# Kernel optimization log

Measured on AMD Instinct MI355X. Metric: run time of the kernel, lower is better.

## Reference

```python
import jax, jax.numpy as jnp
import numpy as np


def _gelu(x):
    # torch F.gelu default = exact (erf) gelu
    return jax.nn.gelu(x, approximate=False)


def _gatv2(x, src, dst, Wl, bl, Wr, br, att, bout, n):
    """PyG GATv2Conv, concat=False (mean over heads), negative_slope=0.2."""
    H, C = att.shape
    xl = (x @ Wl + bl).reshape(n, H, C)  # source-side transform (messages)
    xr = (x @ Wr + br).reshape(n, H, C)  # target-side transform
    e = jax.nn.leaky_relu(xl[src] + xr[dst], 0.2)      # [E,H,C]
    logits = jnp.einsum('ehc,hc->eh', e, att)          # [E,H]
    # segment softmax over incoming edges of each target node
    m = jax.ops.segment_max(logits, dst, num_segments=n)
    m = jnp.where(jnp.isfinite(m), m, 0.0)
    p = jnp.exp(logits - m[dst])
    den = jax.ops.segment_sum(p, dst, num_segments=n)
    alpha = p / (den[dst] + 1e-16)
    out = jax.ops.segment_sum(alpha[:, :, None] * xl[src], dst, num_segments=n)  # [N,H,C]
    return out.mean(axis=1) + bout


def _gnorm(x, w, b, ms):
    """PyG GraphNorm with a single graph (batch == zeros)."""
    mu = x.mean(axis=0, keepdims=True)
    o = x - ms * mu
    var = (o * o).mean(axis=0, keepdims=True)
    return w * o / jnp.sqrt(var + 1e-5) + b


def setup_inputs() -> dict:
    N, E, HID, LAT = 50000, 300000, 128, 256
    key = jax.random.key(0)
    ks = iter(jax.random.split(key, 48))

    def rn(shape, s=0.05):
        return jax.random.normal(next(ks), shape, jnp.float32) * s

    d = {}
    d['z_g'] = rn((1, LAT), 1.0)
    d['edge_index'] = jax.random.randint(next(ks), (2, E), 0, N, dtype=jnp.int32)
    d['template_vertices'] = rn((N, 3), 1.0)
    d['W_ne1'] = rn((3, HID)); d['b_ne1'] = jnp.zeros((HID,))
    d['W_ne2'] = rn((HID, HID)); d['b_ne2'] = jnp.zeros((HID,))
    d['W_s1'] = rn((LAT, HID)); d['b_s1'] = jnp.zeros((HID,))
    d['W_s2'] = rn((HID, HID)); d['b_s2'] = jnp.zeros((HID,))
    for i, h in ((1, 2), (2, 2), (3, 1)):
        d[f'Wl{i}'] = rn((HID, h * HID)); d[f'bl{i}'] = jnp.zeros((h * HID,))
        d[f'Wr{i}'] = rn((HID, h * HID)); d[f'br{i}'] = jnp.zeros((h * HID,))
        d[f'att{i}'] = rn((h, HID)); d[f'bo{i}'] = jnp.zeros((HID,))
        d[f'gn{i}_w'] = jnp.ones((HID,)); d[f'gn{i}_b'] = jnp.zeros((HID,))
        d[f'gn{i}_ms'] = jnp.ones((HID,))
    d['W_h1'] = rn((HID, HID // 2)); d['b_h1'] = jnp.zeros((HID // 2,))
    d['W_h2'] = rn((HID // 2, 3)); d['b_h2'] = jnp.zeros((3,))
    return d


def reference(z_g, edge_index, template_vertices,
              W_ne1, b_ne1, W_ne2, b_ne2, W_s1, b_s1, W_s2, b_s2,
              Wl1, bl1, Wr1, br1, att1, bo1, gn1_w, gn1_b, gn1_ms,
              Wl2, bl2, Wr2, br2, att2, bo2, gn2_w, gn2_b, gn2_ms,
              Wl3, bl3, Wr3, br3, att3, bo3, gn3_w, gn3_b, gn3_ms,
              W_h1, b_h1, W_h2, b_h2):
    n = template_vertices.shape[0]
    sl = jnp.arange(n, dtype=edge_index.dtype)
    src = jnp.concatenate([edge_index[0], sl])  # GATv2Conv add_self_loops=True
    dst = jnp.concatenate([edge_index[1], sl])
    # node embedding + broadcast style (eval mode -> dropout is identity)
    x = _gelu(template_vertices @ W_ne1 + b_ne1) @ W_ne2 + b_ne2
    style = _gelu(z_g @ W_s1 + b_s1) @ W_s2 + b_s2   # [1, hidden]
    x = x + style
    x = _gelu(_gnorm(_gatv2(x, src, dst, Wl1, bl1, Wr1, br1, att1, bo1, n), gn1_w, gn1_b, gn1_ms))
    x = _gelu(_gnorm(_gatv2(x, src, dst, Wl2, bl2, Wr2, br2, att2, bo2, n), gn2_w, gn2_b, gn2_ms))
    x = _gelu(_gnorm(_gatv2(x, src, dst, Wl3, bl3, Wr3, br3, att3, bo3, n), gn3_w, gn3_b, gn3_ms))
    displacement = _gelu(x @ W_h1 + b_h1) @ W_h2 + b_h2   # [n, 3]
    return displacement
```

## Files before the change

kernel.cpp:

```cpp
#include <hip/hip_runtime.h>
#include <hip/hip_fp16.h>
#include <math.h>

#define DEVINL __device__ __forceinline__

using bf16x8 = __attribute__((ext_vector_type(8))) short;
using f32x4  = __attribute__((ext_vector_type(4))) float;
using u16x4  = __attribute__((ext_vector_type(4))) unsigned short;

DEVINL float gelu_f(float v) { return 0.5f * v * (1.0f + erff(v * 0.7071067811865475f)); }
DEVINL float lrelu_f(float v) { return v > 0.0f ? v : 0.2f * v; }
DEVINL unsigned short f2bf(float f) {
    union { float f; unsigned u; } c; c.f = f;
    unsigned r = c.u + 0x7fffu + ((c.u >> 16) & 1u);
    return (unsigned short)(r >> 16);
}
DEVINL float bf2f(unsigned short s) {
    union { unsigned u; float f; } c; c.u = (unsigned)s << 16;
    return c.f;
}
DEVINL unsigned short f2h(float f) {
    __half h = __float2half_rn(f);
    return *(unsigned short*)&h;
}
DEVINL void gl_lds16(const void* g, void* l) {
    __builtin_amdgcn_global_load_lds(
        (const __attribute__((address_space(1))) unsigned*)g,
        (__attribute__((address_space(3))) unsigned*)l, 16, 0, 0);
}
DEVINL void unp8h(const unsigned short* p, float* v) {
    uint4 u = *(const uint4*)p;
    __half2 h0 = *(__half2*)&u.x, h1 = *(__half2*)&u.y;
    __half2 h2 = *(__half2*)&u.z, h3 = *(__half2*)&u.w;
    float2 f0 = __half22float2(h0), f1 = __half22float2(h1);
    float2 f2 = __half22float2(h2), f3 = __half22float2(h3);
    v[0] = f0.x; v[1] = f0.y; v[2] = f1.x; v[3] = f1.y;
    v[4] = f2.x; v[5] = f2.y; v[6] = f3.x; v[7] = f3.y;
}

__global__ void style_k(const float* __restrict__ zg, const float* __restrict__ W1,
                        const float* __restrict__ b1, const float* __restrict__ W2,
                        const float* __restrict__ b2, float* __restrict__ style) {
    __shared__ float s1[128];
    int j = threadIdx.x;
    float a = b1[j];
    for (int k = 0; k < 256; k++) a = fmaf(zg[k], W1[k * 128 + j], a);
    s1[j] = gelu_f(a);
    __syncthreads();
    float o = b2[j];
    for (int k = 0; k < 128; k++) o = fmaf(s1[k], W2[k * 128 + j], o);
    style[j] = o;
}

__global__ void ne1_k(const float* __restrict__ tv, const float* __restrict__ W,
                      const float* __restrict__ b, float* __restrict__ h1, int Nn) {
    int idx = blockIdx.x * blockDim.x + threadIdx.x;
    if (idx >= Nn * 128) return;
    int n = idx >> 7, c = idx & 127;
    float o = fmaf(tv[n * 3 + 0], W[c],
              fmaf(tv[n * 3 + 1], W[128 + c],
              fmaf(tv[n * 3 + 2], W[256 + c], b[c])));
    h1[idx] = gelu_f(o);
}

struct PrepArgs {
    const float* src[8];
    unsigned short* dst;
    int dstoff[8];
    int off[9];
    int shift[8];
};
__global__ void prep_k(PrepArgs a) {
    int idx = blockIdx.x * 256 + threadIdx.x;
    if (idx >= a.off[8]) return;
    int s = 0;
    while (idx >= a.off[s + 1]) s++;
    int e = idx - a.off[s];
    int sh = a.shift[s];
    int k = e >> sh, j = e & ((1 << sh) - 1);
    float w = a.src[s][e];
    unsigned short hi = f2bf(w);
    unsigned short lo = f2bf(w - bf2f(hi));
    int c = j >> 4, lr = j & 15;
    int s2 = k >> 5, lk = (k >> 3) & 3, i = k & 7;
    int lane = lk * 16 + lr;
    size_t base = (size_t)a.dstoff[s] + (size_t)c * 4096 + s2 * 512 + lane * 8 + i;
    a.dst[base] = hi;
    a.dst[base + 2048] = lo;
}

template <int OUT, int EPI, bool DUAL, typename OutT>
__global__ __launch_bounds__(256) void mfma_lin_k(
    const float* __restrict__ xin,
    const unsigned short* __restrict__ WT0, const float* __restrict__ b0,
    const unsigned short* __restrict__ WT1, const float* __restrict__ b1,
    const float* __restrict__ style,
    OutT* __restrict__ out0, OutT* __restrict__ out1, int Nn) {
    constexpr int CPM = OUT / 16;
    constexpr int NCH = (DUAL ? 2 : 1) * CPM;
    __shared__ uint4 buf[2][512];
    int t = threadIdx.x;
    int wave = t >> 6, lane = t & 63;
    int lr = lane & 15, lk = lane >> 4;
    int base = blockIdx.x * 128 + wave * 32;
    int r0 = base + lr, r1 = base + 16 + lr;
    int cr0 = min(r0, Nn - 1), cr1 = min(r1, Nn - 1);

    bf16x8 xh[2][4], xlo[2][4];
#pragma unroll
    for (int rr = 0; rr < 2; rr++) {
        const float* px = xin + (size_t)(rr ? cr1 : cr0) * 128;
#pragma unroll
        for (int s = 0; s < 4; s++) {
            const float4* p4 = (const float4*)(px + s * 32 + lk * 8);
            float4 a = p4[0], b = p4[1];
            float v[8] = {a.x, a.y, a.z, a.w, b.x, b.y, b.z, b.w};
            bf16x8 h, l;
#pragma unroll
            for (int i = 0; i < 8; i++) {
                unsigned short hb = f2bf(v[i]);
                h[i] = (short)hb;
                l[i] = (short)f2bf(v[i] - bf2f(hb));
            }
            xh[rr][s] = h;
            xlo[rr][s] = l;
        }
    }

    auto stage = [&](int c, int bsel) {
        const unsigned short* Wt = (DUAL && c >= CPM) ? WT1 : WT0;
        int cc = (DUAL && c >= CPM) ? c - CPM : c;
        const char* g = (const char*)(Wt + (size_t)cc * 4096);
        char* l = (char*)&buf[bsel][0];
        gl_lds16(g + t * 16, l + wave * 1024);
        gl_lds16(g + 4096 + t * 16, l + 4096 + wave * 1024);
    };

    stage(0, 0);
    for (int c = 0; c < NCH; ++c) {
        int cur = c & 1;
        bool pre = (c + 1 < NCH);
        if (pre) stage(c + 1, cur ^ 1);
        if (pre) asm volatile("s_waitcnt vmcnt(2)" ::: "memory");
        else     asm volatile("s_waitcnt vmcnt(0)" ::: "memory");
        __builtin_amdgcn_s_barrier();

        int m = (DUAL && c >= CPM) ? 1 : 0;
        int j0 = (c - m * CPM) * 16;
        const float* bias = m ? b1 : b0;
        OutT* out = m ? out1 : out0;
        const bf16x8* W = (const bf16x8*)&buf[cur][0];

        f32x4 acc0 = {0.f, 0.f, 0.f, 0.f}, acc1 = {0.f, 0.f, 0.f, 0.f};
#pragma unroll
        for (int s = 0; s < 4; ++s) {
            bf16x8 wh = W[s * 64 + lane];
            bf16x8 wl = W[256 + s * 64 + lane];
            acc0 = __builtin_amdgcn_mfma_f32_16x16x32_bf16(wh, xh[0][s], acc0, 0, 0, 0);
            acc0 = __builtin_amdgcn_mfma_f32_16x16x32_bf16(wh, xlo[0][s], acc0, 0, 0, 0);
            acc0 = __builtin_amdgcn_mfma_f32_16x16x32_bf16(wl, xh[0][s], acc0, 0, 0, 0);
            acc1 = __builtin_amdgcn_mfma_f32_16x16x32_bf16(wh, xh[1][s], acc1, 0, 0, 0);
            acc1 = __builtin_amdgcn_mfma_f32_16x16x32_bf16(wh, xlo[1][s], acc1, 0, 0, 0);
            acc1 = __builtin_amdgcn_mfma_f32_16x16x32_bf16(wl, xh[1][s], acc1, 0, 0, 0);
        }
        int j = j0 + lk * 4;
        float o0[4], o1[4];
#pragma unroll
        for (int i = 0; i < 4; i++) {
            float bb = bias[j + i];
            if (EPI == 1) bb += style[j + i];
            float v0 = acc0[i] + bb, v1 = acc1[i] + bb;
            if (EPI == 2) { v0 = gelu_f(v0); v1 = gelu_f(v1); }
            o0[i] = v0; o1[i] = v1;
        }
        if constexpr (sizeof(OutT) == 2) {
            u16x4 s0 = {f2h(o0[0]), f2h(o0[1]), f2h(o0[2]), f2h(o0[3])};
            u16x4 s1v = {f2h(o1[0]), f2h(o1[1]), f2h(o1[2]), f2h(o1[3])};
            if (r0 < Nn) *(u16x4*)((unsigned short*)out + (size_t)r0 * OUT + j) = s0;
            if (r1 < Nn) *(u16x4*)((unsigned short*)out + (size_t)r1 * OUT + j) = s1v;
        } else {
            if (r0 < Nn) { f32x4 v = {o0[0], o0[1], o0[2], o0[3]}; *(f32x4*)((float*)out + (size_t)r0 * OUT + j) = v; }
            if (r1 < Nn) { f32x4 v = {o1[0], o1[1], o1[2], o1[3]}; *(f32x4*)((float*)out + (size_t)r1 * OUT + j) = v; }
        }
        __builtin_amdgcn_s_barrier();
    }
}

__global__ void count_k(const int* __restrict__ dst, int* __restrict__ counts, int E, int EP) {
    int e = blockIdx.x * blockDim.x + threadIdx.x;
    if (e >= EP) return;
    int d = (e < E) ? dst[e] : (e - E);
    atomicAdd(&counts[d], 1);
}

__global__ void tile_sum_k(const int* __restrict__ counts, int* __restrict__ tsum, int Nn) {
    int i = blockIdx.x * 256 + threadIdx.x;
    int v = (i < Nn) ? counts[i] : 0;
    int lane = threadIdx.x & 63, wave = threadIdx.x >> 6;
#pragma unroll
    for (int off = 1; off < 64; off <<= 1) v += __shfl_xor(v, off, 64);
    __shared__ int red[4];
    if (lane == 0) red[wave] = v;
    __syncthreads();
    if (threadIdx.x == 0) tsum[blockIdx.x] = red[0] + red[1] + red[2] + red[3];
}

__global__ void tile_scan_k(const int* __restrict__ tsum, int* __restrict__ toff,
                            int ntiles, int* __restrict__ rowptr, int Nn, int total) {
    __shared__ int s[256];
    int t = threadIdx.x;
    int v = (t < ntiles) ? tsum[t] : 0;
    s[t] = v;
    __syncthreads();
    for (int off = 1; off < 256; off <<= 1) {
        int a = (t >= off) ? s[t - off] : 0;
        __syncthreads();
        s[t] += a;
        __syncthreads();
    }
    if (t < ntiles) toff[t] = s[t] - v;
    if (t == 0) rowptr[Nn] = total;
}

__global__ void tile_write_k(const int* __restrict__ counts, const int* __restrict__ toff,
                             int* __restrict__ rowptr, int Nn) {
    int i = blockIdx.x * 256 + threadIdx.x;
    int t = threadIdx.x;
    int v = (i < Nn) ? counts[i] : 0;
    __shared__ int s[256];
    s[t] = v;
    __syncthreads();
    for (int off = 1; off < 256; off <<= 1) {
        int a = (t >= off) ? s[t - off] : 0;
        __syncthreads();
        s[t] += a;
        __syncthreads();
    }
    if (i < Nn) rowptr[i] = toff[blockIdx.x] + s[t] - v;
}

__global__ void fill_k(const int* __restrict__ src, const int* __restrict__ dst,
                       const int* __restrict__ rowptr, int* __restrict__ fillc,
                       int* __restrict__ col, int E, int EP) {
    int e = blockIdx.x * blockDim.x + threadIdx.x;
    if (e >= EP) return;
    int d = (e < E) ? dst[e] : (e - E);
    int s = (e < E) ? src[e] : (e - E);
    int pos = atomicAdd(&fillc[d], 1);
    col[rowptr[d] + pos] = s;
}

template <int H>
__global__ __launch_bounds__(256) void gat_gather_k(
    const unsigned short* __restrict__ xl, const unsigned short* __restrict__ xr,
    const float* __restrict__ att, const float* __restrict__ bo,
    const int* __restrict__ rowptr, const int* __restrict__ col,
    float* __restrict__ y, int Nn) {
    constexpr int NPB = (H == 2) ? 2 : 4;
    int w = threadIdx.x >> 6;
    int slot = (H == 2) ? (w >> 1) : w;
    int h = (H == 2) ? (w & 1) : 0;
    int lane = threadIdx.x & 63;
    int g = lane >> 4, sub = lane & 15;
    constexpr int HC = H * 128;
    int n = blockIdx.x * NPB + slot;
    bool act = n < Nn;
    int nn = act ? n : 0;

    float xrv[8], av[8];
    unp8h(xr + (size_t)nn * HC + h * 128 + sub * 8, xrv);
    const float* ap = att + h * 128 + sub * 8;
#pragma unroll
    for (int i = 0; i < 8; i++) av[i] = ap[i];

    float den = 0.f;
    float acc[8] = {0.f, 0.f, 0.f, 0.f, 0.f, 0.f, 0.f, 0.f};
    int beg = act ? rowptr[n] : 0, endp = act ? rowptr[n + 1] : 0;

    for (int k0 = beg; k0 < endp; k0 += 4) {
        int k = k0 + g;
        bool ev = k < endp;
        int s = col[ev ? k : beg];
        float v[8];
        unp8h(xl + (size_t)s * HC + h * 128 + sub * 8, v);
        float p = lrelu_f(v[0] + xrv[0]) * av[0];
#pragma unroll
        for (int i = 1; i < 8; i++) p = fmaf(lrelu_f(v[i] + xrv[i]), av[i], p);
        p += __shfl_xor(p, 1, 64);
        p += __shfl_xor(p, 2, 64);
        p += __shfl_xor(p, 4, 64);
        p += __shfl_xor(p, 8, 64);
        float pe = ev ? __expf(p) : 0.f;
        den += pe;
#pragma unroll
        for (int i = 0; i < 8; i++) acc[i] = fmaf(pe, v[i], acc[i]);
    }
#pragma unroll
    for (int off = 16; off <= 32; off <<= 1) {
        den += __shfl_xor(den, off, 64);
#pragma unroll
        for (int j = 0; j < 8; j++) acc[j] += __shfl_xor(acc[j], off, 64);
    }
    float inv = 1.0f / (den + 1e-16f);

    if constexpr (H == 1) {
        if (act && g == 0) {
            const float* bp = bo + sub * 8;
            f32x4 o0 = {acc[0] * inv + bp[0], acc[1] * inv + bp[1], acc[2] * inv + bp[2], acc[3] * inv + bp[3]};
            f32x4 o1 = {acc[4] * inv + bp[4], acc[5] * inv + bp[5], acc[6] * inv + bp[6], acc[7] * inv + bp[7]};
            *(f32x4*)(y + (size_t)n * 128 + sub * 8) = o0;
            *(f32x4*)(y + (size_t)n * 128 + sub * 8 + 4) = o1;
        }
    } else {
        __shared__ float sh[NPB][2][128];
        if (g == 0) {
#pragma unroll
            for (int j = 0; j < 8; j++) sh[slot][h][sub * 8 + j] = acc[j] * inv;
        }
        __syncthreads();
        int t = threadIdx.x;
        int slot2 = t >> 7, c = t & 127;
        int n2 = blockIdx.x * NPB + slot2;
        if (n2 < Nn)
            y[(size_t)n2 * 128 + c] = (sh[slot2][0][c] + sh[slot2][1][c]) * 0.5f + bo[c];
    }
}

__global__ void gn_stats_k(const float* __restrict__ y, float* __restrict__ stats, int Nn) {
    int c = threadIdx.x;
    int per = (Nn + gridDim.x - 1) / gridDim.x;
    int n0 = blockIdx.x * per, n1 = min(n0 + per, Nn);
    float s = 0.f, s2 = 0.f;
    for (int n = n0; n < n1; n++) {
        float v = y[(size_t)n * 128 + c];
        s += v;
        s2 = fmaf(v, v, s2);
    }
    atomicAdd(&stats[c], s);
    atomicAdd(&stats[128 + c], s2);
}

__global__ void gn_apply_k(const float* __restrict__ y, const float* __restrict__ stats,
                           const float* __restrict__ w, const float* __restrict__ b,
                           const float* __restrict__ ms, float* __restrict__ xo, int Nn) {
    int i4 = blockIdx.x * blockDim.x + threadIdx.x;
    if (i4 >= Nn * 32) return;
    float4 v = reinterpret_cast<const float4*>(y)[i4];
    int c0 = (i4 & 31) * 4;
    float o[4] = {v.x, v.y, v.z, v.w};
    float invN = 1.0f / (float)Nn;
#pragma unroll
    for (int jj = 0; jj < 4; jj++) {
        int c = c0 + jj;
        float mu = stats[c] * invN;
        float ex2 = stats[128 + c] * invN;
        float msv = ms[c];
        float var = ex2 - 2.f * msv * mu * mu + msv * msv * mu * mu;
        float ov = o[jj] - msv * mu;
        float r = rsqrtf(var + 1e-5f);
        o[jj] = gelu_f(fmaf(w[c], ov * r, b[c]));
    }
    float4 res = make_float4(o[0], o[1], o[2], o[3]);
    reinterpret_cast<float4*>(xo)[i4] = res;
}

__global__ void head2_k(const float* __restrict__ h, const float* __restrict__ W,
                        const float* __restrict__ b, float* __restrict__ out, int Nn) {
    __shared__ float w[192];
    __shared__ float bb[3];
    int t = threadIdx.x;
    if (t < 192) w[t] = W[t];
    if (t < 3) bb[t] = b[t];
    __syncthreads();
    int n = blockIdx.x * blockDim.x + t;
    if (n >= Nn) return;
    float a0 = bb[0], a1 = bb[1], a2 = bb[2];
    const float4* h4 = reinterpret_cast<const float4*>(h + (size_t)n * 64);
    for (int k4 = 0; k4 < 16; k4++) {
        float4 v = h4[k4];
        int k = k4 * 4;
        a0 = fmaf(v.x, w[(k + 0) * 3 + 0], a0); a1 = fmaf(v.x, w[(k + 0) * 3 + 1], a1); a2 = fmaf(v.x, w[(k + 0) * 3 + 2], a2);
        a0 = fmaf(v.y, w[(k + 1) * 3 + 0], a0); a1 = fmaf(v.y, w[(k + 1) * 3 + 1], a1); a2 = fmaf(v.y, w[(k + 1) * 3 + 2], a2);
        a0 = fmaf(v.z, w[(k + 2) * 3 + 0], a0); a1 = fmaf(v.z, w[(k + 2) * 3 + 1], a1); a2 = fmaf(v.z, w[(k + 2) * 3 + 2], a2);
        a0 = fmaf(v.w, w[(k + 3) * 3 + 0], a0); a1 = fmaf(v.w, w[(k + 3) * 3 + 1], a1); a2 = fmaf(v.w, w[(k + 3) * 3 + 2], a2);
    }
    out[n * 3 + 0] = a0;
    out[n * 3 + 1] = a1;
    out[n * 3 + 2] = a2;
}

extern "C" void kernel_launch(void* const* d_in, const int* in_sizes, int n_in,
                              void* d_out, int out_size, void* d_ws, size_t ws_size,
                              hipStream_t stream) {
    const float* zg = (const float*)d_in[0];
    const int* ei = (const int*)d_in[1];
    const float* tv = (const float*)d_in[2];
    const float* W_ne1 = (const float*)d_in[3];
    const float* b_ne1 = (const float*)d_in[4];
    const float* W_ne2 = (const float*)d_in[5];
    const float* b_ne2 = (const float*)d_in[6];
    const float* W_s1 = (const float*)d_in[7];
    const float* b_s1 = (const float*)d_in[8];
    const float* W_s2 = (const float*)d_in[9];
    const float* b_s2 = (const float*)d_in[10];
    const float *Wl[3], *bl[3], *Wr[3], *br[3], *attp[3], *bop[3], *gnw[3], *gnb[3], *gnms[3];
    for (int L = 0; L < 3; L++) {
        int base = 11 + L * 9;
        Wl[L] = (const float*)d_in[base + 0];
        bl[L] = (const float*)d_in[base + 1];
        Wr[L] = (const float*)d_in[base + 2];
        br[L] = (const float*)d_in[base + 3];
        attp[L] = (const float*)d_in[base + 4];
        bop[L] = (const float*)d_in[base + 5];
        gnw[L] = (const float*)d_in[base + 6];
        gnb[L] = (const float*)d_in[base + 7];
        gnms[L] = (const float*)d_in[base + 8];
    }
    const float* W_h1 = (const float*)d_in[38];
    const float* b_h1 = (const float*)d_in[39];
    const float* W_h2 = (const float*)d_in[40];
    const float* b_h2 = (const float*)d_in[41];

    int E = in_sizes[1] / 2;
    int N = in_sizes[2] / 3;
    int EP = E + N;
    int NT = (N + 255) / 256;
    const int* srcp = ei;
    const int* dstp = ei + E;

    char* p = (char*)d_ws;
    auto alloc = [&](size_t bytes) -> char* {
        char* r = p;
        p += (bytes + 255) & ~(size_t)255;
        return r;
    };
    float* style = (float*)alloc(512);
    float* h1 = (float*)alloc((size_t)N * 128 * 4);
    float* x = (float*)alloc((size_t)N * 128 * 4);
    unsigned short* xle = (unsigned short*)alloc((size_t)N * 256 * 2);
    unsigned short* xre = (unsigned short*)alloc((size_t)N * 256 * 2);
    float* y = (float*)alloc((size_t)N * 128 * 4);
    float* hb = (float*)alloc((size_t)N * 64 * 4);
    float* stats = (float*)alloc(1024);
    int* rowptr = (int*)alloc(((size_t)N + 1) * 4);
    int* counts = (int*)alloc((size_t)N * 4);
    int* fillc = (int*)alloc((size_t)N * 4);
    int* col = (int*)alloc((size_t)EP * 4);
    int* tsum = (int*)alloc((size_t)NT * 4);
    int* toff = (int*)alloc((size_t)NT * 4);
    unsigned short* wt = (unsigned short*)alloc((size_t)376832 * 2);

    PrepArgs pa;
    const float* srcs[8] = {W_ne2, Wl[0], Wr[0], Wl[1], Wr[1], Wl[2], Wr[2], W_h1};
    int outs[8] = {128, 256, 256, 256, 256, 128, 128, 64};
    int off = 0;
    pa.dst = wt;
    for (int s = 0; s < 8; s++) {
        pa.src[s] = srcs[s];
        pa.off[s] = off;
        pa.dstoff[s] = 2 * off;
        pa.shift[s] = (outs[s] == 256) ? 8 : (outs[s] == 128 ? 7 : 6);
        off += 128 * outs[s];
    }
    pa.off[8] = off;
    const unsigned short* ws_ne2 = wt + pa.dstoff[0];
    const unsigned short* ws_l[3] = {wt + pa.dstoff[1], wt + pa.dstoff[3], wt + pa.dstoff[5]};
    const unsigned short* ws_r[3] = {wt + pa.dstoff[2], wt + pa.dstoff[4], wt + pa.dstoff[6]};
    const unsigned short* ws_h1 = wt + pa.dstoff[7];
    prep_k<<<(off + 255) / 256, 256, 0, stream>>>(pa);

    style_k<<<1, 128, 0, stream>>>(zg, W_s1, b_s1, W_s2, b_s2, style);
    ne1_k<<<(N * 128 + 255) / 256, 256, 0, stream>>>(tv, W_ne1, b_ne1, h1, N);
    mfma_lin_k<128, 1, false, float><<<(N + 127) / 128, 256, 0, stream>>>(
        h1, ws_ne2, b_ne2, nullptr, nullptr, style, x, nullptr, N);

    hipMemsetAsync(counts, 0, (size_t)N * 4, stream);
    hipMemsetAsync(fillc, 0, (size_t)N * 4, stream);
    count_k<<<(EP + 255) / 256, 256, 0, stream>>>(dstp, counts, E, EP);
    tile_sum_k<<<NT, 256, 0, stream>>>(counts, tsum, N);
    tile_scan_k<<<1, 256, 0, stream>>>(tsum, toff, NT, rowptr, N, EP);
    tile_write_k<<<NT, 256, 0, stream>>>(counts, toff, rowptr, N);
    fill_k<<<(EP + 255) / 256, 256, 0, stream>>>(srcp, dstp, rowptr, fillc, col, E, EP);

    const int HS[3] = {2, 2, 1};
    for (int L = 0; L < 3; L++) {
        if (HS[L] == 2) {
            mfma_lin_k<256, 0, true, unsigned short><<<(N + 127) / 128, 256, 0, stream>>>(
                x, ws_l[L], bl[L], ws_r[L], br[L], nullptr, xle, xre, N);
            gat_gather_k<2><<<(N + 1) / 2, 256, 0, stream>>>(xle, xre, attp[L], bop[L], rowptr, col, y, N);
        } else {
            mfma_lin_k<128, 0, true, unsigned short><<<(N + 127) / 128, 256, 0, stream>>>(
                x, ws_l[L], bl[L], ws_r[L], br[L], nullptr, xle, xre, N);
            gat_gather_k<1><<<(N + 3) / 4, 256, 0, stream>>>(xle, xre, attp[L], bop[L], rowptr, col, y, N);
        }
        hipMemsetAsync(stats, 0, 1024, stream);
        gn_stats_k<<<512, 128, 0, stream>>>(y, stats, N);
        gn_apply_k<<<(N * 32 + 255) / 256, 256, 0, stream>>>(y, stats, gnw[L], gnb[L], gnms[L], x, N);
    }

    mfma_lin_k<64, 2, false, float><<<(N + 127) / 128, 256, 0, stream>>>(
        x, ws_h1, b_h1, nullptr, nullptr, nullptr, hb, nullptr, N);
    head2_k<<<(N + 255) / 256, 256, 0, stream>>>(hb, W_h2, b_h2, (float*)d_out, N);
}
```

Before: 677.3 us.

## Use packed fp16 math in GAT gather and fold memsets into kernels

The attention score in the gather kernel is now computed with packed half2 add, leaky-relu via max, and fdot2 accumulation, instead of unpacking to fp32 and running scalar FMAs. The separate hipMemsetAsync calls for counts, fill counters and GraphNorm stats are removed, and those buffers are zeroed inside kernels that already run earlier (ne1, tile_write, gather block 0). This cuts ALU work in the hot gather loop and removes several tiny launches. In exchange, the logit sum of lrelu(xl+xr) is formed at fp16 precision, and the stats zeroing in gather block 0 is safe only because gn_stats runs after the gather kernel.

```diff
diff --git a/kernel.cpp b/kernel.cpp
--- a/kernel.cpp
+++ b/kernel.cpp
@@ -7,6 +7,7 @@
 using bf16x8 = __attribute__((ext_vector_type(8))) short;
 using f32x4  = __attribute__((ext_vector_type(4))) float;
 using u16x4  = __attribute__((ext_vector_type(4))) unsigned short;
+using f16x2  = __attribute__((ext_vector_type(2))) _Float16;
 
 DEVINL float gelu_f(float v) { return 0.5f * v * (1.0f + erff(v * 0.7071067811865475f)); }
 DEVINL float lrelu_f(float v) { return v > 0.0f ? v : 0.2f * v; }
@@ -23,19 +24,13 @@
     __half h = __float2half_rn(f);
     return *(unsigned short*)&h;
 }
+DEVINL f16x2 b2h2(unsigned u) {
+    union { unsigned u; f16x2 h; } c; c.u = u; return c.h;
+}
 DEVINL void gl_lds16(const void* g, void* l) {
     __builtin_amdgcn_global_load_lds(
         (const __attribute__((address_space(1))) unsigned*)g,
         (__attribute__((address_space(3))) unsigned*)l, 16, 0, 0);
-}
-DEVINL void unp8h(const unsigned short* p, float* v) {
-    uint4 u = *(const uint4*)p;
-    __half2 h0 = *(__half2*)&u.x, h1 = *(__half2*)&u.y;
-    __half2 h2 = *(__half2*)&u.z, h3 = *(__half2*)&u.w;
-    float2 f0 = __half22float2(h0), f1 = __half22float2(h1);
-    float2 f2 = __half22float2(h2), f3 = __half22float2(h3);
-    v[0] = f0.x; v[1] = f0.y; v[2] = f1.x; v[3] = f1.y;
-    v[4] = f2.x; v[5] = f2.y; v[6] = f3.x; v[7] = f3.y;
 }
 
 __global__ void style_k(const float* __restrict__ zg, const float* __restrict__ W1,
@@ -53,8 +48,10 @@
 }
 
 __global__ void ne1_k(const float* __restrict__ tv, const float* __restrict__ W,
-                      const float* __restrict__ b, float* __restrict__ h1, int Nn) {
+                      const float* __restrict__ b, float* __restrict__ h1,
+                      int* __restrict__ counts, int Nn) {
     int idx = blockIdx.x * blockDim.x + threadIdx.x;
+    if (idx < Nn) counts[idx] = 0;
     if (idx >= Nn * 128) return;
     int n = idx >> 7, c = idx & 127;
     float o = fmaf(tv[n * 3 + 0], W[c],
@@ -223,10 +220,11 @@
 }
 
 __global__ void tile_write_k(const int* __restrict__ counts, const int* __restrict__ toff,
-                             int* __restrict__ rowptr, int Nn) {
+                             int* __restrict__ rowptr, int* __restrict__ fillc, int Nn) {
     int i = blockIdx.x * 256 + threadIdx.x;
     int t = threadIdx.x;
     int v = (i < Nn) ? counts[i] : 0;
+    if (i < Nn) fillc[i] = 0;
     __shared__ int s[256];
     s[t] = v;
     __syncthreads();
@@ -255,7 +253,8 @@
     const unsigned short* __restrict__ xl, const unsigned short* __restrict__ xr,
     const float* __restrict__ att, const float* __restrict__ bo,
     const int* __restrict__ rowptr, const int* __restrict__ col,
-    float* __restrict__ y, int Nn) {
+    float* __restrict__ y, float* __restrict__ stats, int Nn) {
+    if (blockIdx.x == 0 && threadIdx.x < 256) stats[threadIdx.x] = 0.f;
     constexpr int NPB = (H == 2) ? 2 : 4;
     int w = threadIdx.x >> 6;
     int slot = (H == 2) ? (w >> 1) : w;
@@ -267,11 +266,16 @@
     bool act = n < Nn;
     int nn = act ? n : 0;
 
-    float xrv[8], av[8];
-    unp8h(xr + (size_t)nn * HC + h * 128 + sub * 8, xrv);
+    uint4 uxr = *(const uint4*)(xr + (size_t)nn * HC + h * 128 + sub * 8);
+    f16x2 xrv[4] = {b2h2(uxr.x), b2h2(uxr.y), b2h2(uxr.z), b2h2(uxr.w)};
     const float* ap = att + h * 128 + sub * 8;
-#pragma unroll
-    for (int i = 0; i < 8; i++) av[i] = ap[i];
+    f16x2 a2[4];
+#pragma unroll
+    for (int i = 0; i < 4; i++) {
+        f16x2 t; t.x = (_Float16)ap[2 * i]; t.y = (_Float16)ap[2 * i + 1];
+        a2[i] = t;
+    }
+    f16x2 c02; c02.x = (_Float16)0.2f; c02.y = (_Float16)0.2f;
 
     float den = 0.f;
     float acc[8] = {0.f, 0.f, 0.f, 0.f, 0.f, 0.f, 0.f, 0.f};
@@ -281,11 +285,20 @@
         int k = k0 + g;
         bool ev = k < endp;
         int s = col[ev ? k : beg];
-        float v[8];
-        unp8h(xl + (size_t)s * HC + h * 128 + sub * 8, v);
-        float p = lrelu_f(v[0] + xrv[0]) * av[0];
-#pragma unroll
-        for (int i = 1; i < 8; i++) p = fmaf(lrelu_f(v[i] + xrv[i]), av[i], p);
+        uint4 u = *(const uint4*)(xl + (size_t)s * HC + h * 128 + sub * 8);
+        f16x2 v2[4] = {b2h2(u.x), b2h2(u.y), b2h2(u.z), b2h2(u.w)};
+        float p = 0.f;
+#pragma unroll
+        for (int i = 0; i < 4; i++) {
+            f16x2 t = v2[i] + xrv[i];
+            f16x2 e = __builtin_elementwise_max(t, t * c02);
+#if __has_builtin(__builtin_amdgcn_fdot2)
+            p = __builtin_amdgcn_fdot2(e, a2[i], p, false);
+#else
+            p = fmaf((float)e.x, (float)a2[i].x, p);
+            p = fmaf((float)e.y, (float)a2[i].y, p);
+#endif
+        }
         p += __shfl_xor(p, 1, 64);
         p += __shfl_xor(p, 2, 64);
         p += __shfl_xor(p, 4, 64);
@@ -293,7 +306,10 @@
         float pe = ev ? __expf(p) : 0.f;
         den += pe;
 #pragma unroll
-        for (int i = 0; i < 8; i++) acc[i] = fmaf(pe, v[i], acc[i]);
+        for (int i = 0; i < 4; i++) {
+            acc[2 * i]     = fmaf(pe, (float)v2[i].x, acc[2 * i]);
+            acc[2 * i + 1] = fmaf(pe, (float)v2[i].y, acc[2 * i + 1]);
+        }
     }
 #pragma unroll
     for (int off = 16; off <= 32; off <<= 1) {
@@ -470,16 +486,14 @@
     prep_k<<<(off + 255) / 256, 256, 0, stream>>>(pa);
 
     style_k<<<1, 128, 0, stream>>>(zg, W_s1, b_s1, W_s2, b_s2, style);
-    ne1_k<<<(N * 128 + 255) / 256, 256, 0, stream>>>(tv, W_ne1, b_ne1, h1, N);
+    ne1_k<<<(N * 128 + 255) / 256, 256, 0, stream>>>(tv, W_ne1, b_ne1, h1, counts, N);
     mfma_lin_k<128, 1, false, float><<<(N + 127) / 128, 256, 0, stream>>>(
         h1, ws_ne2, b_ne2, nullptr, nullptr, style, x, nullptr, N);
 
-    hipMemsetAsync(counts, 0, (size_t)N * 4, stream);
-    hipMemsetAsync(fillc, 0, (size_t)N * 4, stream);
     count_k<<<(EP + 255) / 256, 256, 0, stream>>>(dstp, counts, E, EP);
     tile_sum_k<<<NT, 256, 0, stream>>>(counts, tsum, N);
     tile_scan_k<<<1, 256, 0, stream>>>(tsum, toff, NT, rowptr, N, EP);
-    tile_write_k<<<NT, 256, 0, stream>>>(counts, toff, rowptr, N);
+    tile_write_k<<<NT, 256, 0, stream>>>(counts, toff, rowptr, fillc, N);
     fill_k<<<(EP + 255) / 256, 256, 0, stream>>>(srcp, dstp, rowptr, fillc, col, E, EP);
 
     const int HS[3] = {2, 2, 1};
@@ -487,13 +501,12 @@
         if (HS[L] == 2) {
             mfma_lin_k<256, 0, true, unsigned short><<<(N + 127) / 128, 256, 0, stream>>>(
                 x, ws_l[L], bl[L], ws_r[L], br[L], nullptr, xle, xre, N);
-            gat_gather_k<2><<<(N + 1) / 2, 256, 0, stream>>>(xle, xre, attp[L], bop[L], rowptr, col, y, N);
+            gat_gather_k<2><<<(N + 1) / 2, 256, 0, stream>>>(xle, xre, attp[L], bop[L], rowptr, col, y, stats, N);
         } else {
             mfma_lin_k<128, 0, true, unsigned short><<<(N + 127) / 128, 256, 0, stream>>>(
                 x, ws_l[L], bl[L], ws_r[L], br[L], nullptr, xle, xre, N);
-            gat_gather_k<1><<<(N + 3) / 4, 256, 0, stream>>>(xle, xre, attp[L], bop[L], rowptr, col, y, N);
-        }
-        hipMemsetAsync(stats, 0, 1024, stream);
+            gat_gather_k<1><<<(N + 3) / 4, 256, 0, stream>>>(xle, xre, attp[L], bop[L], rowptr, col, y, stats, N);
+        }
         gn_stats_k<<<512, 128, 0, stream>>>(y, stats, N);
         gn_apply_k<<<(N * 32 + 255) / 256, 256, 0, stream>>>(y, stats, gnw[L], gnb[L], gnms[L], x, N);
     }
```

New measurement: 667.0 us. No clear change (-1.5%).
